# Performance work log

Hardware: AMD Instinct MI355X
Metric: run time of the kernel (lower is better)

Reference implementation:

```python
import jax, jax.numpy as jnp
import numpy as np

D_MODEL = 1024
N_HEADS = 16
HEAD_DIM = D_MODEL // N_HEADS


def setup_inputs() -> dict:
    key = jax.random.key(0)
    k1, k2, k3, k4, k5 = jax.random.split(key, 5)
    s = 1.0 / np.sqrt(D_MODEL)
    return {
        "x": jax.random.normal(k1, (2, 2048, D_MODEL), dtype=jnp.float32),
        "w_qkv": jax.random.normal(k2, (D_MODEL, 3 * D_MODEL), dtype=jnp.float32) * s,
        "b_qkv": jax.random.normal(k3, (3 * D_MODEL,), dtype=jnp.float32) * 0.02,
        "w_proj": jax.random.normal(k4, (D_MODEL, D_MODEL), dtype=jnp.float32) * s,
        "b_proj": jax.random.normal(k5, (D_MODEL,), dtype=jnp.float32) * 0.02,
    }


def reference(x, w_qkv, b_qkv, w_proj, b_proj):
    B, S, D = x.shape
    H, Hd = N_HEADS, HEAD_DIM
    qkv = x @ w_qkv + b_qkv                       # [B,S,3D]
    q, k, v = jnp.split(qkv, 3, axis=-1)
    # split heads -> [B,H,S,Hd]
    q = q.reshape(B, S, H, Hd).transpose(0, 2, 1, 3)
    k = k.reshape(B, S, H, Hd).transpose(0, 2, 1, 3)
    v = v.reshape(B, S, H, Hd).transpose(0, 2, 1, 3)
    scale = 1.0 / jnp.sqrt(jnp.asarray(Hd, dtype=x.dtype))
    scores = jnp.einsum("bhqd,bhkd->bhqk", q, k) * scale  # [B,H,S,S]
    causal = jnp.tril(jnp.ones((S, S), dtype=bool))
    scores = jnp.where(causal, scores, jnp.asarray(-jnp.inf, dtype=scores.dtype))
    attn = jax.nn.softmax(scores, axis=-1)
    out = jnp.einsum("bhqk,bhkd->bhqd", attn, v)  # [B,H,S,Hd]
    out = out.transpose(0, 2, 1, 3).reshape(B, S, D)
    return out @ w_proj + b_proj
```

## Files before the change

### kernel.cpp

```cpp
#include <hip/hip_runtime.h>


typedef float f32x4 __attribute__((ext_vector_type(4)));
typedef short bf16x8 __attribute__((ext_vector_type(8)));

#if __has_builtin(__builtin_amdgcn_exp2f)
#define EXP2(x) __builtin_amdgcn_exp2f(x)
#else
#define EXP2(x) exp2f(x)
#endif

__device__ __forceinline__ unsigned short f2bf(float f) {
  union { float f; unsigned u; } v; v.f = f;
  unsigned u = v.u + 0x7fffu + ((v.u >> 16) & 1u);
  return (unsigned short)(u >> 16);
}

__device__ __forceinline__ unsigned pack2bf(float f0, float f1) {
  union { float f; unsigned u; } a, b;
  a.f = f1; b.f = f0;
  return __builtin_amdgcn_perm(a.u + 0x8000u, b.u + 0x8000u, 0x07060302u);
}

__device__ __forceinline__ void async_load16(const void* g, void* lds) {
  __builtin_amdgcn_global_load_lds(
      (const __attribute__((address_space(1))) void*)g,
      (__attribute__((address_space(3))) void*)lds, 16, 0, 0);
}

__global__ void f32_to_bf16_kernel(const float* __restrict__ in,
                                   unsigned short* __restrict__ out, int n) {
  int i = (blockIdx.x * 256 + threadIdx.x) * 4;
  if (i < n) {
    float4 f = *(const float4*)(in + i);
    ushort4 o;
    o.x = f2bf(f.x); o.y = f2bf(f.y); o.z = f2bf(f.z); o.w = f2bf(f.w);
    *(ushort4*)(out + i) = o;
  }
}

__global__ void transpose_f32_bf16_kernel(const float* __restrict__ in,
                                          unsigned short* __restrict__ out,
                                          int K, int N) {
  __shared__ float tile[32][33];
  int n0 = blockIdx.x * 32, k0 = blockIdx.y * 32;
  int tx = threadIdx.x, ty = threadIdx.y;
#pragma unroll
  for (int i = ty; i < 32; i += 8)
    tile[i][tx] = in[(size_t)(k0 + i) * N + (n0 + tx)];
  __syncthreads();
#pragma unroll
  for (int i = ty; i < 32; i += 8)
    out[(size_t)(n0 + i) * K + (k0 + tx)] = f2bf(tile[tx][i]);
}

template <int MI, int NI>
__device__ __forceinline__ void gemm_mainloop(
    const unsigned short* __restrict__ A,
    const unsigned short* __restrict__ BT,
    int K, int mBlk, int nBlk,
    unsigned short* As, unsigned short* Bs,
    f32x4 (&acc)[MI][NI], int lane, int wave)
{
  const int l16 = lane & 15, quad = lane >> 4;
  const int mW = (wave >> 1) * MI * 16;
  const int nW = (wave & 1) * NI * 16;
  constexpr int AROWS = 2 * MI * 16;
  constexpr int BROWS = 2 * NI * 16;
  constexpr int AINST = AROWS / 64;
  constexpr int BINST = BROWS / 64;
  const int rl = lane >> 2;
  const int cl = (lane & 3) * 8;

  for (int k0 = 0; k0 < K; k0 += 32) {
    __syncthreads();
#pragma unroll
    for (int t = 0; t < AINST; ++t) {
      const int rbase = wave * (AROWS / 4) + t * 16;
      async_load16(A + (size_t)(mBlk + rbase + rl) * K + k0 + cl, &As[rbase * 32]);
    }
#pragma unroll
    for (int t = 0; t < BINST; ++t) {
      const int rbase = wave * (BROWS / 4) + t * 16;
      async_load16(BT + (size_t)(nBlk + rbase + rl) * K + k0 + cl, &Bs[rbase * 32]);
    }
    __syncthreads();

    bf16x8 af[MI], bf[NI];
#pragma unroll
    for (int i = 0; i < MI; ++i)
      af[i] = *(const bf16x8*)&As[(mW + i * 16 + l16) * 32 + quad * 8];
#pragma unroll
    for (int j = 0; j < NI; ++j)
      bf[j] = *(const bf16x8*)&Bs[(nW + j * 16 + l16) * 32 + quad * 8];
#pragma unroll
    for (int i = 0; i < MI; ++i)
#pragma unroll
      for (int j = 0; j < NI; ++j)
        acc[i][j] = __builtin_amdgcn_mfma_f32_16x16x32_bf16(af[i], bf[j], acc[i][j], 0, 0, 0);
  }
}

__global__ __launch_bounds__(256) void qkv_gemm_kernel(
    const unsigned short* __restrict__ A,
    const unsigned short* __restrict__ WT,
    const float* __restrict__ bias,
    unsigned short* __restrict__ QKV)
{
  __shared__ unsigned short As[128 * 32];
  __shared__ unsigned short Bs[128 * 32];
  const int lane = threadIdx.x & 63;
  const int wave = threadIdx.x >> 6;
  const int l16 = lane & 15, quad = lane >> 4;

  f32x4 acc[4][4];
  const f32x4 z4 = {0.f, 0.f, 0.f, 0.f};
#pragma unroll
  for (int i = 0; i < 4; ++i)
#pragma unroll
    for (int j = 0; j < 4; ++j) acc[i][j] = z4;

  gemm_mainloop<4, 4>(A, WT, 1024, blockIdx.x * 128, blockIdx.y * 128,
                      As, Bs, acc, lane, wave);

  const int m0 = blockIdx.x * 128 + (wave >> 1) * 64;
  const int n0 = blockIdx.y * 128 + (wave & 1) * 64;
  const int whichW = n0 >> 10;
  const int bb = m0 >> 11;
  const int sBase = (m0 & 2047);
  const size_t planeE = (size_t)2 * 16 * 2048 * 64;

  if (whichW == 2) {
    unsigned short* Vb = QKV + 2 * planeE;
#pragma unroll
    for (int j = 0; j < 4; ++j) {
      const int rem = (n0 & 1023) + j * 16 + l16;
      const int hh = rem >> 6, hd = rem & 63;
      const float bv = bias[n0 + j * 16 + l16];
      unsigned short* col = Vb + (((size_t)bb * 16 + hh) * 64 + hd) * 2048;
#pragma unroll
      for (int i = 0; i < 4; ++i) {
        unsigned short pk[4];
#pragma unroll
        for (int r = 0; r < 4; ++r) pk[r] = f2bf(acc[i][j][r] + bv);
        *(ushort4*)&col[sBase + i * 16 + quad * 4] = *(ushort4*)pk;
      }
    }
  } else {
    const float scale = (whichW == 0) ? 0.18033688011112042f : 1.0f;
#pragma unroll
    for (int j = 0; j < 4; ++j) {
      const int n = n0 + j * 16 + l16;
      const float bv = bias[n];
      const int rem = n & 1023;
      const int hh = rem >> 6, hd = rem & 63;
      unsigned short* pl = QKV + (size_t)whichW * planeE +
                           (((size_t)bb * 16 + hh) * 2048) * 64 + hd;
#pragma unroll
      for (int r = 0; r < 4; ++r) {
        const int s = sBase + (quad * 4 + r);
#pragma unroll
        for (int i = 0; i < 4; ++i)
          pl[(size_t)(s + i * 16) * 64] = f2bf((acc[i][j][r] + bv) * scale);
      }
    }
  }
}

__global__ __launch_bounds__(256) void attn_kernel(
    const unsigned short* __restrict__ QKV,
    unsigned short* __restrict__ AO)
{
  __shared__ __align__(16) unsigned short Ks[3 * 64 * 64];
  __shared__ __align__(16) unsigned short Vs[3 * 64 * 64];
  __shared__ unsigned short Plds[4 * 32 * 72];
  const int lane = threadIdx.x & 63;
  const int wave = threadIdx.x >> 6;
  const int l16 = lane & 15, quad = lane >> 4;
  const int h = blockIdx.y, b = blockIdx.z;
  const int qg = b ? blockIdx.x : (15 - blockIdx.x);
  const int qw = qg * 128 + wave * 32;

  const size_t planeE = (size_t)2 * 16 * 2048 * 64;
  const size_t bhS = ((size_t)b * 16 + h) * (size_t)(2048 * 64);
  const unsigned short* Q   = QKV + bhS;
  const unsigned short* Kg  = QKV + planeE + bhS;
  const unsigned short* VTg = QKV + 2 * planeE + bhS;

  unsigned short* Pw = Plds + wave * (32 * 72);
  const f32x4 z4 = {0.f, 0.f, 0.f, 0.f};

  bf16x8 qf_[2][2];
#pragma unroll
  for (int qf = 0; qf < 2; ++qf)
#pragma unroll
    for (int hf = 0; hf < 2; ++hf)
      qf_[qf][hf] = *(const bf16x8*)(Q + (size_t)(qw + qf * 16 + l16) * 64 + hf * 32 + quad * 8);

  f32x4 O[2][4];
#pragma unroll
  for (int qf = 0; qf < 2; ++qf)
#pragma unroll
    for (int f = 0; f < 4; ++f) O[qf][f] = z4;
  float lpa[2] = {0.f, 0.f}, lpb[2] = {0.f, 0.f};

  const int tbase = (wave & 1) * 4;
  const bool doV = wave >= 2;
  const int sw7 = l16 & 7;

  auto stage = [&](int tileIdx, int bufIdx) {
    const int kt = tileIdx * 64;
    unsigned short* Kb = Ks + bufIdx * 4096;
    unsigned short* Vb = Vs + bufIdx * 4096;
#pragma unroll
    for (int i = 0; i < 4; ++i) {
      const int t = tbase + i;
      const int s = t * 64 + lane;
      const int row = s >> 3;
      const int c = (s & 7) ^ (row & 7);
      if (doV)
        async_load16(VTg + (size_t)row * 2048 + kt + c * 8, Vb + t * 512);
      else
        async_load16(Kg + (size_t)(kt + row) * 64 + c * 8, Kb + t * 512);
    }
  };

  const int nt = qg * 2 + 2;
  stage(0, 0);
  stage(1, 1);
  for (int ti = 0; ti < nt; ++ti) {
    asm volatile("s_waitcnt vmcnt(4)\n\ts_barrier" ::: "memory");
    const int tn = (ti + 2 < nt) ? ti + 2 : nt - 1;
    stage(tn, (ti + 2) % 3);
    const int kt = ti * 64;
    const unsigned short* Kb = Ks + (ti % 3) * 4096;
    const unsigned short* Vb = Vs + (ti % 3) * 4096;

    if (kt <= qw + 31) {
      const bool dmask = (kt + 63 > qw);
      f32x4 sc[4][2];
#pragma unroll
      for (int kg = 0; kg < 4; ++kg) {
        const int row = kg * 16 + l16;
        bf16x8 ka0 = *(const bf16x8*)&Kb[(row * 8 + (quad ^ sw7)) * 8];
        bf16x8 ka1 = *(const bf16x8*)&Kb[(row * 8 + ((4 + quad) ^ sw7)) * 8];
#pragma unroll
        for (int qf = 0; qf < 2; ++qf) {
          f32x4 s0 = z4;
          s0 = __builtin_amdgcn_mfma_f32_16x16x32_bf16(ka0, qf_[qf][0], s0, 0, 0, 0);
          s0 = __builtin_amdgcn_mfma_f32_16x16x32_bf16(ka1, qf_[qf][1], s0, 0, 0, 0);
          sc[kg][qf] = s0;
        }
      }

#pragma unroll
      for (int kg = 0; kg < 4; ++kg)
#pragma unroll
        for (int qf = 0; qf < 2; ++qf) {
          float p[4];
#pragma unroll
          for (int r = 0; r < 4; ++r) {
            float v = sc[kg][qf][r];
            if (dmask) {
              const int key = kt + kg * 16 + quad * 4 + r;
              const int q = qw + qf * 16 + l16;
              if (key > q) v = -INFINITY;
            }
            p[r] = EXP2(v);
          }
          lpa[qf] += p[0] + p[1];
          lpb[qf] += p[2] + p[3];
          uint2 pk;
          pk.x = pack2bf(p[0], p[1]);
          pk.y = pack2bf(p[2], p[3]);
          *(uint2*)&Pw[(qf * 16 + l16) * 72 + kg * 16 + quad * 4] = pk;
        }
      asm volatile("s_waitcnt lgkmcnt(0)" ::: "memory");

#pragma unroll
      for (int ks = 0; ks < 2; ++ks) {
        bf16x8 pa[2];
#pragma unroll
        for (int qf = 0; qf < 2; ++qf)
          pa[qf] = *(const bf16x8*)&Pw[(qf * 16 + l16) * 72 + ks * 32 + quad * 8];
#pragma unroll
        for (int f = 0; f < 4; ++f) {
          const int row = f * 16 + l16;
          bf16x8 vb = *(const bf16x8*)&Vb[(row * 8 + ((ks * 4 + quad) ^ sw7)) * 8];
#pragma unroll
          for (int qf = 0; qf < 2; ++qf)
            O[qf][f] = __builtin_amdgcn_mfma_f32_16x16x32_bf16(pa[qf], vb, O[qf][f], 0, 0, 0);
        }
      }
    }
  }

  float lp[2] = {lpa[0] + lpb[0], lpa[1] + lpb[1]};
#pragma unroll
  for (int qf = 0; qf < 2; ++qf) {
    lp[qf] += __shfl_xor(lp[qf], 16, 64);
    lp[qf] += __shfl_xor(lp[qf], 32, 64);
  }

#pragma unroll
  for (int qf = 0; qf < 2; ++qf) {
    float inv[4];
#pragma unroll
    for (int r = 0; r < 4; ++r)
      inv[r] = 1.0f / __shfl(lp[qf], quad * 4 + r, 64);
    unsigned short* op = AO + ((size_t)b * 2048 + qw + qf * 16 + quad * 4) * 1024 + h * 64 + l16;
#pragma unroll
    for (int f = 0; f < 4; ++f)
#pragma unroll
      for (int r = 0; r < 4; ++r)
        op[(size_t)r * 1024 + f * 16] = f2bf(O[qf][f][r] * inv[r]);
  }
}

__global__ __launch_bounds__(256) void proj_gemm_kernel(
    const unsigned short* __restrict__ A,
    const unsigned short* __restrict__ WT,
    const float* __restrict__ bias,
    float* __restrict__ out)
{
  __shared__ unsigned short As[64 * 32];
  __shared__ unsigned short Bs[128 * 32];
  const int lane = threadIdx.x & 63;
  const int wave = threadIdx.x >> 6;
  const int l16 = lane & 15, quad = lane >> 4;

  f32x4 acc[2][4];
  const f32x4 z4 = {0.f, 0.f, 0.f, 0.f};
#pragma unroll
  for (int i = 0; i < 2; ++i)
#pragma unroll
    for (int j = 0; j < 4; ++j) acc[i][j] = z4;

  gemm_mainloop<2, 4>(A, WT, 1024, blockIdx.x * 64, blockIdx.y * 128,
                      As, Bs, acc, lane, wave);

  const int m0 = blockIdx.x * 64 + (wave >> 1) * 32;
  const int n0 = blockIdx.y * 128 + (wave & 1) * 64;
#pragma unroll
  for (int i = 0; i < 2; ++i) {
#pragma unroll
    for (int j = 0; j < 4; ++j) {
      const int n = n0 + j * 16 + l16;
      const float bv = bias[n];
#pragma unroll
      for (int r = 0; r < 4; ++r) {
        const int m = m0 + i * 16 + quad * 4 + r;
        out[(size_t)m * 1024 + n] = acc[i][j][r] + bv;
      }
    }
  }
}

extern "C" void kernel_launch(void* const* d_in, const int* in_sizes, int n_in,
                              void* d_out, int out_size, void* d_ws, size_t ws_size,
                              hipStream_t stream) {
  const float* x      = (const float*)d_in[0];
  const float* w_qkv  = (const float*)d_in[1];
  const float* b_qkv  = (const float*)d_in[2];
  const float* w_proj = (const float*)d_in[3];
  const float* b_proj = (const float*)d_in[4];
  float* out = (float*)d_out;

  unsigned short* Xb  = (unsigned short*)d_ws;
  unsigned short* WTq = Xb + (size_t)4096 * 1024;
  unsigned short* WTp = WTq + (size_t)3072 * 1024;
  unsigned short* QKV = WTp + (size_t)1024 * 1024;
  unsigned short* AO  = QKV + (size_t)3 * 4096 * 1024;

  f32_to_bf16_kernel<<<4096, 256, 0, stream>>>(x, Xb, 4096 * 1024);
  transpose_f32_bf16_kernel<<<dim3(96, 32), dim3(32, 8), 0, stream>>>(w_qkv, WTq, 1024, 3072);
  transpose_f32_bf16_kernel<<<dim3(32, 32), dim3(32, 8), 0, stream>>>(w_proj, WTp, 1024, 1024);
  qkv_gemm_kernel<<<dim3(32, 24), 256, 0, stream>>>(Xb, WTq, b_qkv, QKV);
  attn_kernel<<<dim3(16, 16, 2), 256, 0, stream>>>(QKV, AO);
  proj_gemm_kernel<<<dim3(64, 8), 256, 0, stream>>>(AO, WTp, b_proj, out);
}
```

Before: 204.8 us.

## Triple-buffer GEMM mainloops, software-pipeline PV MFMAs, merge weight transposes

The shared GEMM mainloop moves from a single-buffered load/sync loop to a three-stage async LDS ring with vmcnt-based waits, so global loads for tile k+2 overlap compute on tile k. The attention kernel delays the P·V MFMAs by one tile, issuing them alongside the next tile's K fragment loads and QK^T to hide LDS latency, with a trailing drain step. The two weight-transpose launches are merged into one kernel to save a launch. In exchange, LDS use and register pressure go up, which can lower occupancy.

```diff
diff --git a/kernel.cpp b/kernel.cpp
--- a/kernel.cpp
+++ b/kernel.cpp
@@ -39,11 +39,18 @@
   }
 }
 
-__global__ void transpose_f32_bf16_kernel(const float* __restrict__ in,
-                                          unsigned short* __restrict__ out,
-                                          int K, int N) {
+__global__ void transpose_weights_kernel(const float* __restrict__ wqkv,
+                                         const float* __restrict__ wproj,
+                                         unsigned short* __restrict__ WTq,
+                                         unsigned short* __restrict__ WTp) {
   __shared__ float tile[32][33];
-  int n0 = blockIdx.x * 32, k0 = blockIdx.y * 32;
+  const int K = 1024;
+  const float* in;
+  unsigned short* out;
+  int N, nx;
+  if (blockIdx.x < 96) { in = wqkv; out = WTq; N = 3072; nx = blockIdx.x; }
+  else                 { in = wproj; out = WTp; N = 1024; nx = blockIdx.x - 96; }
+  int n0 = nx * 32, k0 = blockIdx.y * 32;
   int tx = threadIdx.x, ty = threadIdx.y;
 #pragma unroll
   for (int i = ty; i < 32; i += 8)
@@ -69,30 +76,46 @@
   constexpr int BROWS = 2 * NI * 16;
   constexpr int AINST = AROWS / 64;
   constexpr int BINST = BROWS / 64;
+  constexpr int ASZ = AROWS * 32;
+  constexpr int BSZ = BROWS * 32;
   const int rl = lane >> 2;
   const int cl = (lane & 3) * 8;
 
-  for (int k0 = 0; k0 < K; k0 += 32) {
-    __syncthreads();
+  auto stage = [&](int k0, int buf) {
 #pragma unroll
     for (int t = 0; t < AINST; ++t) {
       const int rbase = wave * (AROWS / 4) + t * 16;
-      async_load16(A + (size_t)(mBlk + rbase + rl) * K + k0 + cl, &As[rbase * 32]);
+      async_load16(A + (size_t)(mBlk + rbase + rl) * K + k0 + cl,
+                   &As[buf * ASZ + rbase * 32]);
     }
 #pragma unroll
     for (int t = 0; t < BINST; ++t) {
       const int rbase = wave * (BROWS / 4) + t * 16;
-      async_load16(BT + (size_t)(nBlk + rbase + rl) * K + k0 + cl, &Bs[rbase * 32]);
-    }
-    __syncthreads();
+      async_load16(BT + (size_t)(nBlk + rbase + rl) * K + k0 + cl,
+                   &Bs[buf * BSZ + rbase * 32]);
+    }
+  };
+
+  const int kiters = K / 32;
+  stage(0, 0);
+  stage(32, 1);
+  for (int it = 0; it < kiters; ++it) {
+    if constexpr (AINST + BINST == 4)
+      asm volatile("s_waitcnt vmcnt(4)\n\ts_barrier" ::: "memory");
+    else
+      asm volatile("s_waitcnt vmcnt(3)\n\ts_barrier" ::: "memory");
+    const int kn = (it + 2 < kiters) ? (it + 2) * 32 : (kiters - 1) * 32;
+    stage(kn, (it + 2) % 3);
+    const unsigned short* Ab = As + (it % 3) * ASZ;
+    const unsigned short* Bb = Bs + (it % 3) * BSZ;
 
     bf16x8 af[MI], bf[NI];
 #pragma unroll
     for (int i = 0; i < MI; ++i)
-      af[i] = *(const bf16x8*)&As[(mW + i * 16 + l16) * 32 + quad * 8];
+      af[i] = *(const bf16x8*)&Ab[(mW + i * 16 + l16) * 32 + quad * 8];
 #pragma unroll
     for (int j = 0; j < NI; ++j)
-      bf[j] = *(const bf16x8*)&Bs[(nW + j * 16 + l16) * 32 + quad * 8];
+      bf[j] = *(const bf16x8*)&Bb[(nW + j * 16 + l16) * 32 + quad * 8];
 #pragma unroll
     for (int i = 0; i < MI; ++i)
 #pragma unroll
@@ -107,8 +130,8 @@
     const float* __restrict__ bias,
     unsigned short* __restrict__ QKV)
 {
-  __shared__ unsigned short As[128 * 32];
-  __shared__ unsigned short Bs[128 * 32];
+  __shared__ unsigned short As[3 * 128 * 32];
+  __shared__ unsigned short Bs[3 * 128 * 32];
   const int lane = threadIdx.x & 63;
   const int wave = threadIdx.x >> 6;
   const int l16 = lane & 15, quad = lane >> 4;
@@ -225,7 +248,11 @@
     }
   };
 
+  bf16x8 paP[2][2];
+  bf16x8 vbP[2][4];
   const int nt = qg * 2 + 2;
+  const int C = qg * 2 + (wave >> 1) + 1;
+
   stage(0, 0);
   stage(1, 1);
   for (int ti = 0; ti < nt; ++ti) {
@@ -235,23 +262,38 @@
     const int kt = ti * 64;
     const unsigned short* Kb = Ks + (ti % 3) * 4096;
     const unsigned short* Vb = Vs + (ti % 3) * 4096;
-
-    if (kt <= qw + 31) {
+    const bool comp = ti < C;
+
+    bf16x8 ka[4][2];
+    if (comp) {
+#pragma unroll
+      for (int kg = 0; kg < 4; ++kg) {
+        const int row = kg * 16 + l16;
+        ka[kg][0] = *(const bf16x8*)&Kb[(row * 8 + (quad ^ sw7)) * 8];
+        ka[kg][1] = *(const bf16x8*)&Kb[(row * 8 + ((4 + quad) ^ sw7)) * 8];
+      }
+    }
+    if (ti >= 1 && ti <= C) {
+#pragma unroll
+      for (int ks = 0; ks < 2; ++ks)
+#pragma unroll
+        for (int f = 0; f < 4; ++f)
+#pragma unroll
+          for (int qf = 0; qf < 2; ++qf)
+            O[qf][f] = __builtin_amdgcn_mfma_f32_16x16x32_bf16(paP[ks][qf], vbP[ks][f], O[qf][f], 0, 0, 0);
+    }
+    if (comp) {
       const bool dmask = (kt + 63 > qw);
       f32x4 sc[4][2];
 #pragma unroll
-      for (int kg = 0; kg < 4; ++kg) {
-        const int row = kg * 16 + l16;
-        bf16x8 ka0 = *(const bf16x8*)&Kb[(row * 8 + (quad ^ sw7)) * 8];
-        bf16x8 ka1 = *(const bf16x8*)&Kb[(row * 8 + ((4 + quad) ^ sw7)) * 8];
+      for (int kg = 0; kg < 4; ++kg)
 #pragma unroll
         for (int qf = 0; qf < 2; ++qf) {
           f32x4 s0 = z4;
-          s0 = __builtin_amdgcn_mfma_f32_16x16x32_bf16(ka0, qf_[qf][0], s0, 0, 0, 0);
-          s0 = __builtin_amdgcn_mfma_f32_16x16x32_bf16(ka1, qf_[qf][1], s0, 0, 0, 0);
+          s0 = __builtin_amdgcn_mfma_f32_16x16x32_bf16(ka[kg][0], qf_[qf][0], s0, 0, 0, 0);
+          s0 = __builtin_amdgcn_mfma_f32_16x16x32_bf16(ka[kg][1], qf_[qf][1], s0, 0, 0, 0);
           sc[kg][qf] = s0;
         }
-      }
 
 #pragma unroll
       for (int kg = 0; kg < 4; ++kg)
@@ -279,20 +321,25 @@
 
 #pragma unroll
       for (int ks = 0; ks < 2; ++ks) {
-        bf16x8 pa[2];
 #pragma unroll
         for (int qf = 0; qf < 2; ++qf)
-          pa[qf] = *(const bf16x8*)&Pw[(qf * 16 + l16) * 72 + ks * 32 + quad * 8];
+          paP[ks][qf] = *(const bf16x8*)&Pw[(qf * 16 + l16) * 72 + ks * 32 + quad * 8];
 #pragma unroll
         for (int f = 0; f < 4; ++f) {
           const int row = f * 16 + l16;
-          bf16x8 vb = *(const bf16x8*)&Vb[(row * 8 + ((ks * 4 + quad) ^ sw7)) * 8];
-#pragma unroll
-          for (int qf = 0; qf < 2; ++qf)
-            O[qf][f] = __builtin_amdgcn_mfma_f32_16x16x32_bf16(pa[qf], vb, O[qf][f], 0, 0, 0);
+          vbP[ks][f] = *(const bf16x8*)&Vb[(row * 8 + ((ks * 4 + quad) ^ sw7)) * 8];
         }
       }
     }
+  }
+  if (C == nt) {
+#pragma unroll
+    for (int ks = 0; ks < 2; ++ks)
+#pragma unroll
+      for (int f = 0; f < 4; ++f)
+#pragma unroll
+        for (int qf = 0; qf < 2; ++qf)
+          O[qf][f] = __builtin_amdgcn_mfma_f32_16x16x32_bf16(paP[ks][qf], vbP[ks][f], O[qf][f], 0, 0, 0);
   }
 
   float lp[2] = {lpa[0] + lpb[0], lpa[1] + lpb[1]};
@@ -323,8 +370,8 @@
     const float* __restrict__ bias,
     float* __restrict__ out)
 {
-  __shared__ unsigned short As[64 * 32];
-  __shared__ unsigned short Bs[128 * 32];
+  __shared__ unsigned short As[3 * 64 * 32];
+  __shared__ unsigned short Bs[3 * 128 * 32];
   const int lane = threadIdx.x & 63;
   const int wave = threadIdx.x >> 6;
   const int l16 = lane & 15, quad = lane >> 4;
@@ -373,8 +420,7 @@
   unsigned short* AO  = QKV + (size_t)3 * 4096 * 1024;
 
   f32_to_bf16_kernel<<<4096, 256, 0, stream>>>(x, Xb, 4096 * 1024);
-  transpose_f32_bf16_kernel<<<dim3(96, 32), dim3(32, 8), 0, stream>>>(w_qkv, WTq, 1024, 3072);
-  transpose_f32_bf16_kernel<<<dim3(32, 32), dim3(32, 8), 0, stream>>>(w_proj, WTp, 1024, 1024);
+  transpose_weights_kernel<<<dim3(128, 32), dim3(32, 8), 0, stream>>>(w_qkv, w_proj, WTq, WTp);
   qkv_gemm_kernel<<<dim3(32, 24), 256, 0, stream>>>(Xb, WTq, b_qkv, QKV);
   attn_kernel<<<dim3(16, 16, 2), 256, 0, stream>>>(QKV, AO);
   proj_gemm_kernel<<<dim3(64, 8), 256, 0, stream>>>(AO, WTp, b_proj, out);
```

Measured after the change: 211.2 us. 3.1% more time.
